# Performance work log

Measured on AMD Instinct MI355X. Metric: run time of the kernel, lower is better.

## Reference

```python
import math
import jax, jax.numpy as jnp
import numpy as np

B, N, DQ, DK, DV, H = 8, 1024, 256, 256, 256, 8
EPS_SM = 1e-15
EPS_LN = 1e-5


def _layer_norm(x, g, b):
    mu = jnp.mean(x, axis=-1, keepdims=True)
    var = jnp.mean((x - mu) ** 2, axis=-1, keepdims=True)
    return (x - mu) * jax.lax.rsqrt(var + EPS_LN) * g + b


def setup_inputs() -> dict:
    key = jax.random.key(0)
    ks = jax.random.split(key, 16)
    s = 0.05
    inp = {
        "Q": jax.random.normal(ks[0], (B, N, DQ), jnp.float32),
        "K": jax.random.normal(ks[1], (B, N, DK), jnp.float32),
        "lengths": jnp.clip(jax.random.randint(ks[2], (B,), 0, N), 1, N),
        "Wq": jax.random.normal(ks[3], (DQ, DV), jnp.float32) * s,
        "bq": jnp.zeros((DV,), jnp.float32),
        "Wk": jax.random.normal(ks[4], (DK, DV), jnp.float32) * s,
        "bk": jnp.zeros((DV,), jnp.float32),
        "Wv": jax.random.normal(ks[5], (DK, DV), jnp.float32) * s,
        "bv": jnp.zeros((DV,), jnp.float32),
        "Wo": jax.random.normal(ks[6], (DV, DV), jnp.float32) * s,
        "bo": jnp.zeros((DV,), jnp.float32),
        "g0": jnp.ones((DV,), jnp.float32),
        "b0": jnp.zeros((DV,), jnp.float32),
        "g1": jnp.ones((DV,), jnp.float32),
        "b1": jnp.zeros((DV,), jnp.float32),
    }
    return inp


def reference(Q, K, lengths, Wq, bq, Wk, bk, Wv, bv, Wo, bo, g0, b0, g1, b1):
    d = DV // H  # head dim
    mask = (jnp.arange(N) < lengths[:, None]).astype(Q.dtype)  # (B, N)
    q = (Q @ Wq + bq) * mask[..., None]  # (B, N, DV)
    k = (K @ Wk + bk) * mask[..., None]
    v = (K @ Wv + bv) * mask[..., None]
    qh = q.reshape(B, N, H, d)
    kh = k.reshape(B, N, H, d)
    vh = v.reshape(B, N, H, d)
    # NB: original scales by sqrt(dim_V), not sqrt(head_dim)
    scores = jnp.einsum("bnhd,bmhd->bhnm", qh, kh) / math.sqrt(DV)
    # set_softmax: raw exp, mask rows and cols by lengths, normalize over keys
    e = jnp.exp(scores) * mask[:, None, :, None] * mask[:, None, None, :]
    A = e / (jnp.sum(e, axis=-1, keepdims=True) + EPS_SM)  # (B, H, N, N)
    O = qh + jnp.einsum("bhnm,bmhd->bnhd", A, vh)  # residual per head
    O = O.reshape(B, N, DV)
    O = _layer_norm(O, g0, b0)
    O = O + jax.nn.relu(O @ Wo + bo)
    O = _layer_norm(O, g1, b1)
    return O
```

## Files before the change

kernel.cpp:

```cpp
#include <hip/hip_runtime.h>
#include <hip/hip_bf16.h>


typedef __attribute__((ext_vector_type(8))) short short8;
typedef __attribute__((ext_vector_type(4))) short short4v;
typedef __attribute__((ext_vector_type(4))) float f32x4;

__device__ __forceinline__ short f2bf(float f) {
    union { float f; unsigned u; } x; x.f = f;
    unsigned r = x.u + 0x7fffu + ((x.u >> 16) & 1u);
    return (short)(r >> 16);
}
__device__ __forceinline__ float bf2f(short s) {
    union { unsigned u; float f; } x; x.u = ((unsigned)(unsigned short)s) << 16;
    return x.f;
}

__global__ __launch_bounds__(256) void wtrans_kernel(
    const float* __restrict__ Wq, const float* __restrict__ Wk,
    const float* __restrict__ Wv, const float* __restrict__ Wo,
    short* __restrict__ WqT, short* __restrict__ WkT,
    short* __restrict__ WvT, short* __restrict__ WoT)
{
    __shared__ short tile[64][72];
    const float* W; short* T;
    switch (blockIdx.y) {
        case 0:  W = Wq; T = WqT; break;
        case 1:  W = Wk; T = WkT; break;
        case 2:  W = Wv; T = WvT; break;
        default: W = Wo; T = WoT; break;
    }
    const int k0 = (blockIdx.x >> 2) * 64;
    const int n0 = (blockIdx.x & 3) * 64;
    const int c  = threadIdx.x & 63;
    const int r4 = threadIdx.x >> 6;
    #pragma unroll
    for (int i = 0; i < 16; i++) {
        int k = r4 + i * 4;
        tile[k][c] = f2bf(W[(size_t)(k0 + k) * 256 + n0 + c]);
    }
    __syncthreads();
    #pragma unroll
    for (int i = 0; i < 16; i++) {
        int n = r4 + i * 4;
        T[(size_t)(n0 + n) * 256 + k0 + c] = tile[c][n];
    }
}

__global__ __launch_bounds__(256) void proj_kernel(
    const float* __restrict__ Q, const float* __restrict__ Kin,
    const short* __restrict__ WqT, const short* __restrict__ WkT, const short* __restrict__ WvT,
    const float* __restrict__ bq, const float* __restrict__ bk, const float* __restrict__ bv,
    const int* __restrict__ lengths,
    short* __restrict__ qb, short* __restrict__ kb, short* __restrict__ vT)
{
    __shared__ short Xt[32][264];
    const int which = blockIdx.y;
    const float* A   = (which == 0) ? Q   : Kin;
    const short* WTa = (which == 0) ? WqT : WkT;

    const int tid = threadIdx.x;
    const int b = blockIdx.x >> 5;
    const int len = lengths[b];
    const int r0b = blockIdx.x * 32;
    const int ntok0b = r0b & 1023;

    if (ntok0b < len) {
        #pragma unroll
        for (int it = 0; it < 8; it++) {
            int e = tid + it * 256;
            int row = e >> 6, c4 = (e & 63) * 4;
            float4 f = *(const float4*)(A + (size_t)(r0b + row) * 256 + c4);
            short4v s4;
            s4[0] = f2bf(f.x); s4[1] = f2bf(f.y); s4[2] = f2bf(f.z); s4[3] = f2bf(f.w);
            *(short4v*)(&Xt[row][c4]) = s4;
        }
    }
    __syncthreads();

    const int lane = tid & 63, wid = tid >> 6;
    const int m = lane & 15, quad = lane >> 4;
    const int rh = wid >> 1, ch = wid & 1;
    const int c0 = ch * 128;
    const int ntok0 = ntok0b + rh * 16;

    f32x4 accA[8], accB[8];
    #pragma unroll
    for (int t = 0; t < 8; t++) {
        accA[t] = (f32x4){0.f, 0.f, 0.f, 0.f};
        accB[t] = (f32x4){0.f, 0.f, 0.f, 0.f};
    }

    if (ntok0 < len) {
        for (int kk = 0; kk < 256; kk += 32) {
            short8 af = *(const short8*)(&Xt[rh * 16 + m][kk + quad * 8]);
            #pragma unroll
            for (int t = 0; t < 8; t++) {
                short8 bfa = *(const short8*)(WTa + (c0 + t * 16 + m) * 256 + kk + quad * 8);
                accA[t] = __builtin_amdgcn_mfma_f32_16x16x32_bf16(af, bfa, accA[t], 0, 0, 0);
            }
            if (which == 1) {
                #pragma unroll
                for (int t = 0; t < 8; t++) {
                    short8 bfb = *(const short8*)(WvT + (c0 + t * 16 + m) * 256 + kk + quad * 8);
                    accB[t] = __builtin_amdgcn_mfma_f32_16x16x32_bf16(af, bfb, accB[t], 0, 0, 0);
                }
            }
        }
    }

    const float KSCALE = 0.0625f;
    #pragma unroll
    for (int t = 0; t < 8; t++) {
        int n = c0 + t * 16 + m;
        int h = n >> 5, i = n & 31;
        int bh = b * 8 + h;
        if (which == 0) {
            float bias = bq[n];
            #pragma unroll
            for (int reg = 0; reg < 4; reg++) {
                int ntok = ntok0 + quad * 4 + reg;
                float val = (ntok < len) ? (accA[t][reg] + bias) : 0.f;
                qb[((size_t)bh * 1024 + ntok) * 32 + i] = f2bf(val);
            }
        } else {
            float bk_ = bk[n];
            float bv_ = bv[n];
            #pragma unroll
            for (int reg = 0; reg < 4; reg++) {
                int ntok = ntok0 + quad * 4 + reg;
                bool ok = ntok < len;
                float vk = ok ? (accA[t][reg] + bk_) * KSCALE : 0.f;
                float vv = ok ? (accB[t][reg] + bv_) : 0.f;
                kb[((size_t)bh * 1024 + ntok) * 32 + i] = f2bf(vk);
                vT[(size_t)(bh * 32 + i) * 1024 + ntok] = f2bf(vv);
            }
        }
    }
}

__global__ __launch_bounds__(256) void attn_kernel(
    const short* __restrict__ qb, const short* __restrict__ kb, const short* __restrict__ vT,
    const int* __restrict__ lengths, float* __restrict__ O1)
{
    __shared__ short Kb[2][64][36];
    __shared__ short Vb[2][32][76];
    __shared__ short P[4][16][72];
    const int tid = threadIdx.x;
    const int lane = tid & 63, wid = tid >> 6;
    const int m = lane & 15, quad = lane >> 4;
    const int bh = blockIdx.y;
    const int b = bh >> 3, h = bh & 7;
    const int len = lengths[b];
    const int qr0 = blockIdx.x * 64 + wid * 16;
    const bool active = qr0 < len;

    const short* qbase = qb + (size_t)bh * 1024 * 32;
    const short* kbase = kb + (size_t)bh * 1024 * 32;
    const short* vbase = vT + (size_t)bh * 32 * 1024;

    const short8 qf = *(const short8*)(qbase + (qr0 + m) * 32 + quad * 8);

    f32x4 o0 = (f32x4){0.f, 0.f, 0.f, 0.f};
    f32x4 o1 = (f32x4){0.f, 0.f, 0.f, 0.f};
    float l[4] = {0.f, 0.f, 0.f, 0.f};

    const int nch = (blockIdx.x * 64 < len) ? ((len + 63) >> 6) : 0;

    short8 kr, vr;
    if (nch > 0) {
        kr = *(const short8*)(kbase + tid * 8);
        vr = *(const short8*)(vbase + (size_t)(tid >> 3) * 1024 + (tid & 7) * 8);
    }

    for (int ci = 0; ci < nch; ci++) {
        const int buf = ci & 1;
        *(short8*)(&Kb[buf][tid >> 2][(tid & 3) * 8]) = kr;
        *(short8*)(&Vb[buf][tid >> 3][(tid & 7) * 8]) = vr;
        if (ci + 1 < nch) {
            int k1 = (ci + 1) * 64;
            kr = *(const short8*)(kbase + k1 * 32 + tid * 8);
            vr = *(const short8*)(vbase + (size_t)(tid >> 3) * 1024 + k1 + (tid & 7) * 8);
        }
        __syncthreads();

        if (active) {
            const int key0 = ci * 64;
            #pragma unroll
            for (int t = 0; t < 4; t++) {
                short8 kf = *(const short8*)(&Kb[buf][t * 16 + m][quad * 8]);
                f32x4 s = __builtin_amdgcn_mfma_f32_16x16x32_bf16(qf, kf,
                            (f32x4){0.f, 0.f, 0.f, 0.f}, 0, 0, 0);
                int col = key0 + t * 16 + m;
                bool cm = col < len;
                #pragma unroll
                for (int reg = 0; reg < 4; reg++) {
                    float e = cm ? __expf(s[reg]) : 0.f;
                    l[reg] += e;
                    P[wid][quad * 4 + reg][t * 16 + m] = f2bf(e);
                }
            }
            asm volatile("s_waitcnt lgkmcnt(0)" ::: "memory");
            #pragma unroll
            for (int c = 0; c < 2; c++) {
                short8 pf  = *(const short8*)(&P[wid][m][c * 32 + quad * 8]);
                short8 vf0 = *(const short8*)(&Vb[buf][m][c * 32 + quad * 8]);
                short8 vf1 = *(const short8*)(&Vb[buf][16 + m][c * 32 + quad * 8]);
                o0 = __builtin_amdgcn_mfma_f32_16x16x32_bf16(pf, vf0, o0, 0, 0, 0);
                o1 = __builtin_amdgcn_mfma_f32_16x16x32_bf16(pf, vf1, o1, 0, 0, 0);
            }
        }
    }

    #pragma unroll
    for (int reg = 0; reg < 4; reg++) {
        float s = l[reg];
        s += __shfl_xor(s, 1); s += __shfl_xor(s, 2);
        s += __shfl_xor(s, 4); s += __shfl_xor(s, 8);
        l[reg] = s;
    }

    const int hbase = h * 32;
    #pragma unroll
    for (int reg = 0; reg < 4; reg++) {
        int qrow = qr0 + quad * 4 + reg;
        float f = (qrow < len) ? 1.f / (l[reg] + 1e-15f) : 0.f;
        size_t obase = ((size_t)(b * 1024 + qrow)) * 256 + hbase;
        float q0 = bf2f(qbase[qrow * 32 + m]);
        float q1 = bf2f(qbase[qrow * 32 + 16 + m]);
        O1[obase + m]      = q0 + o0[reg] * f;
        O1[obase + 16 + m] = q1 + o1[reg] * f;
    }
}

__global__ __launch_bounds__(256) void out_kernel(
    const float* __restrict__ O1, const short* __restrict__ WoT,
    const float* __restrict__ g0, const float* __restrict__ b0,
    const float* __restrict__ bo, const float* __restrict__ g1, const float* __restrict__ b1,
    float* __restrict__ out)
{
    __shared__ short Xs[16][264];
    __shared__ float st[4][2][16];
    const int tid = threadIdx.x;
    const int r0 = blockIdx.x * 16;

    {
        const int lrow  = tid >> 4;
        const int cbase = (tid & 15) * 16;
        const float* rowp = O1 + (size_t)(r0 + lrow) * 256 + cbase;
        float4 a0 = ((const float4*)rowp)[0];
        float4 a1 = ((const float4*)rowp)[1];
        float4 a2 = ((const float4*)rowp)[2];
        float4 a3 = ((const float4*)rowp)[3];
        float s  = a0.x + a0.y + a0.z + a0.w + a1.x + a1.y + a1.z + a1.w
                 + a2.x + a2.y + a2.z + a2.w + a3.x + a3.y + a3.z + a3.w;
        float s2 = a0.x*a0.x + a0.y*a0.y + a0.z*a0.z + a0.w*a0.w
                 + a1.x*a1.x + a1.y*a1.y + a1.z*a1.z + a1.w*a1.w
                 + a2.x*a2.x + a2.y*a2.y + a2.z*a2.z + a2.w*a2.w
                 + a3.x*a3.x + a3.y*a3.y + a3.z*a3.z + a3.w*a3.w;
        s  += __shfl_xor(s, 1);  s  += __shfl_xor(s, 2);
        s  += __shfl_xor(s, 4);  s  += __shfl_xor(s, 8);
        s2 += __shfl_xor(s2, 1); s2 += __shfl_xor(s2, 2);
        s2 += __shfl_xor(s2, 4); s2 += __shfl_xor(s2, 8);
        float mean = s * (1.f / 256.f);
        float var  = s2 * (1.f / 256.f) - mean * mean;
        float rs = rsqrtf(var + 1e-5f);
        float4 g0a = ((const float4*)(g0 + cbase))[0];
        float4 g0b = ((const float4*)(g0 + cbase))[1];
        float4 g0c = ((const float4*)(g0 + cbase))[2];
        float4 g0d = ((const float4*)(g0 + cbase))[3];
        float4 b0a = ((const float4*)(b0 + cbase))[0];
        float4 b0b = ((const float4*)(b0 + cbase))[1];
        float4 b0c = ((const float4*)(b0 + cbase))[2];
        float4 b0d = ((const float4*)(b0 + cbase))[3];
        short8 y0, y1;
        y0[0] = f2bf((a0.x - mean) * rs * g0a.x + b0a.x);
        y0[1] = f2bf((a0.y - mean) * rs * g0a.y + b0a.y);
        y0[2] = f2bf((a0.z - mean) * rs * g0a.z + b0a.z);
        y0[3] = f2bf((a0.w - mean) * rs * g0a.w + b0a.w);
        y0[4] = f2bf((a1.x - mean) * rs * g0b.x + b0b.x);
        y0[5] = f2bf((a1.y - mean) * rs * g0b.y + b0b.y);
        y0[6] = f2bf((a1.z - mean) * rs * g0b.z + b0b.z);
        y0[7] = f2bf((a1.w - mean) * rs * g0b.w + b0b.w);
        y1[0] = f2bf((a2.x - mean) * rs * g0c.x + b0c.x);
        y1[1] = f2bf((a2.y - mean) * rs * g0c.y + b0c.y);
        y1[2] = f2bf((a2.z - mean) * rs * g0c.z + b0c.z);
        y1[3] = f2bf((a2.w - mean) * rs * g0c.w + b0c.w);
        y1[4] = f2bf((a3.x - mean) * rs * g0d.x + b0d.x);
        y1[5] = f2bf((a3.y - mean) * rs * g0d.y + b0d.y);
        y1[6] = f2bf((a3.z - mean) * rs * g0d.z + b0d.z);
        y1[7] = f2bf((a3.w - mean) * rs * g0d.w + b0d.w);
        *(short8*)(&Xs[lrow][cbase])     = y0;
        *(short8*)(&Xs[lrow][cbase + 8]) = y1;
    }
    __syncthreads();

    const int lane = tid & 63, wid = tid >> 6;
    const int m = lane & 15, quad = lane >> 4;
    const int c0 = wid * 64;

    f32x4 acc[4];
    #pragma unroll
    for (int t = 0; t < 4; t++) acc[t] = (f32x4){0.f, 0.f, 0.f, 0.f};

    for (int kk = 0; kk < 256; kk += 32) {
        short8 af = *(const short8*)(&Xs[m][kk + quad * 8]);
        #pragma unroll
        for (int t = 0; t < 4; t++) {
            short8 bf = *(const short8*)(WoT + (c0 + t * 16 + m) * 256 + kk + quad * 8);
            acc[t] = __builtin_amdgcn_mfma_f32_16x16x32_bf16(af, bf, acc[t], 0, 0, 0);
        }
    }

    float s1[4] = {0.f, 0.f, 0.f, 0.f};
    float s2v[4] = {0.f, 0.f, 0.f, 0.f};
    #pragma unroll
    for (int t = 0; t < 4; t++) {
        int n = c0 + t * 16 + m;
        float bon = bo[n];
        #pragma unroll
        for (int reg = 0; reg < 4; reg++) {
            int r = quad * 4 + reg;
            float xv = bf2f(Xs[r][n]);
            float c = acc[t][reg] + bon;
            float yv = xv + (c > 0.f ? c : 0.f);
            acc[t][reg] = yv;
            s1[reg] += yv;
            s2v[reg] += yv * yv;
        }
    }
    #pragma unroll
    for (int reg = 0; reg < 4; reg++) {
        float a = s1[reg], bsum = s2v[reg];
        a += __shfl_xor(a, 1); a += __shfl_xor(a, 2); a += __shfl_xor(a, 4); a += __shfl_xor(a, 8);
        bsum += __shfl_xor(bsum, 1); bsum += __shfl_xor(bsum, 2); bsum += __shfl_xor(bsum, 4); bsum += __shfl_xor(bsum, 8);
        s1[reg] = a; s2v[reg] = bsum;
    }
    if (m == 0) {
        #pragma unroll
        for (int reg = 0; reg < 4; reg++) {
            st[wid][0][quad * 4 + reg] = s1[reg];
            st[wid][1][quad * 4 + reg] = s2v[reg];
        }
    }
    __syncthreads();
    #pragma unroll
    for (int reg = 0; reg < 4; reg++) {
        int r = quad * 4 + reg;
        float t1 = st[0][0][r] + st[1][0][r] + st[2][0][r] + st[3][0][r];
        float t2 = st[0][1][r] + st[1][1][r] + st[2][1][r] + st[3][1][r];
        float mean = t1 * (1.f / 256.f);
        float var  = t2 * (1.f / 256.f) - mean * mean;
        float rs = rsqrtf(var + 1e-5f);
        int token = r0 + r;
        #pragma unroll
        for (int t = 0; t < 4; t++) {
            int n = c0 + t * 16 + m;
            out[(size_t)token * 256 + n] = (acc[t][reg] - mean) * rs * g1[n] + b1[n];
        }
    }
}

extern "C" void kernel_launch(void* const* d_in, const int* in_sizes, int n_in,
                              void* d_out, int out_size, void* d_ws, size_t ws_size,
                              hipStream_t stream) {
    const float* Q   = (const float*)d_in[0];
    const float* K   = (const float*)d_in[1];
    const int* lengths = (const int*)d_in[2];
    const float* Wq  = (const float*)d_in[3];
    const float* bq  = (const float*)d_in[4];
    const float* Wk  = (const float*)d_in[5];
    const float* bk  = (const float*)d_in[6];
    const float* Wv  = (const float*)d_in[7];
    const float* bv  = (const float*)d_in[8];
    const float* Wo  = (const float*)d_in[9];
    const float* bo  = (const float*)d_in[10];
    const float* g0  = (const float*)d_in[11];
    const float* b0  = (const float*)d_in[12];
    const float* g1  = (const float*)d_in[13];
    const float* b1  = (const float*)d_in[14];
    float* out = (float*)d_out;

    char* ws = (char*)d_ws;
    short* qb  = (short*)(ws);
    short* kb  = (short*)(ws + (4u << 20));
    short* vT  = (short*)(ws + (8u << 20));
    float* O1  = (float*)(ws + (12u << 20));
    short* WqT = (short*)(ws + (20u << 20));
    short* WkT = (short*)(ws + (20u << 20) + (128u << 10));
    short* WvT = (short*)(ws + (20u << 20) + (256u << 10));
    short* WoT = (short*)(ws + (20u << 20) + (384u << 10));

    wtrans_kernel<<<dim3(16, 4), 256, 0, stream>>>(Wq, Wk, Wv, Wo, WqT, WkT, WvT, WoT);
    proj_kernel<<<dim3(256, 2), 256, 0, stream>>>(Q, K, WqT, WkT, WvT, bq, bk, bv,
                                                  lengths, qb, kb, vT);
    attn_kernel<<<dim3(16, 64), 256, 0, stream>>>(qb, kb, vT, lengths, O1);
    out_kernel<<<dim3(512), 256, 0, stream>>>(O1, WoT, g0, b0, bo, g1, b1, out);
}
```

Before: 150.7 us.

## Double rows per warp in attention and output kernels to reuse K/V and Wo

The attention kernel now has each warp handle 32 query rows (two 16-row tiles) instead of 16, so each block covers 128 queries and every staged K/V chunk is reused across twice as many rows, halving the grid. The output kernel likewise processes 32 tokens per block, reusing each Wo fragment for two MFMA row tiles. This cuts redundant global loads of K/V and Wo and the number of blocks, at the cost of more registers per thread and less parallelism (512 attention blocks, 256 output blocks), which may hurt occupancy and load balance for short sequences.

```diff
diff --git a/kernel.cpp b/kernel.cpp
--- a/kernel.cpp
+++ b/kernel.cpp
@@ -145,27 +145,30 @@
 {
     __shared__ short Kb[2][64][36];
     __shared__ short Vb[2][32][76];
-    __shared__ short P[4][16][72];
+    __shared__ short P[4][2][16][72];
     const int tid = threadIdx.x;
     const int lane = tid & 63, wid = tid >> 6;
     const int m = lane & 15, quad = lane >> 4;
     const int bh = blockIdx.y;
     const int b = bh >> 3, h = bh & 7;
     const int len = lengths[b];
-    const int qr0 = blockIdx.x * 64 + wid * 16;
-    const bool active = qr0 < len;
+    const int qr0 = blockIdx.x * 128 + wid * 32;
+    const bool act0 = qr0 < len;
+    const bool act1 = qr0 + 16 < len;
 
     const short* qbase = qb + (size_t)bh * 1024 * 32;
     const short* kbase = kb + (size_t)bh * 1024 * 32;
     const short* vbase = vT + (size_t)bh * 32 * 1024;
 
-    const short8 qf = *(const short8*)(qbase + (qr0 + m) * 32 + quad * 8);
-
-    f32x4 o0 = (f32x4){0.f, 0.f, 0.f, 0.f};
-    f32x4 o1 = (f32x4){0.f, 0.f, 0.f, 0.f};
-    float l[4] = {0.f, 0.f, 0.f, 0.f};
-
-    const int nch = (blockIdx.x * 64 < len) ? ((len + 63) >> 6) : 0;
+    const short8 qf0 = *(const short8*)(qbase + (qr0 + m) * 32 + quad * 8);
+    const short8 qf1 = *(const short8*)(qbase + (qr0 + 16 + m) * 32 + quad * 8);
+
+    f32x4 o00 = (f32x4){0.f,0.f,0.f,0.f}, o01 = (f32x4){0.f,0.f,0.f,0.f};
+    f32x4 o10 = (f32x4){0.f,0.f,0.f,0.f}, o11 = (f32x4){0.f,0.f,0.f,0.f};
+    float l0[4] = {0.f,0.f,0.f,0.f};
+    float l1[4] = {0.f,0.f,0.f,0.f};
+
+    const int nch = (blockIdx.x * 128 < len) ? ((len + 63) >> 6) : 0;
 
     short8 kr, vr;
     if (nch > 0) {
@@ -184,52 +187,91 @@
         }
         __syncthreads();
 
-        if (active) {
-            const int key0 = ci * 64;
+        const int key0 = ci * 64;
+        if (act0) {
             #pragma unroll
             for (int t = 0; t < 4; t++) {
                 short8 kf = *(const short8*)(&Kb[buf][t * 16 + m][quad * 8]);
-                f32x4 s = __builtin_amdgcn_mfma_f32_16x16x32_bf16(qf, kf,
+                f32x4 s = __builtin_amdgcn_mfma_f32_16x16x32_bf16(qf0, kf,
                             (f32x4){0.f, 0.f, 0.f, 0.f}, 0, 0, 0);
                 int col = key0 + t * 16 + m;
                 bool cm = col < len;
                 #pragma unroll
                 for (int reg = 0; reg < 4; reg++) {
                     float e = cm ? __expf(s[reg]) : 0.f;
-                    l[reg] += e;
-                    P[wid][quad * 4 + reg][t * 16 + m] = f2bf(e);
+                    l0[reg] += e;
+                    P[wid][0][quad * 4 + reg][t * 16 + m] = f2bf(e);
                 }
             }
             asm volatile("s_waitcnt lgkmcnt(0)" ::: "memory");
             #pragma unroll
             for (int c = 0; c < 2; c++) {
-                short8 pf  = *(const short8*)(&P[wid][m][c * 32 + quad * 8]);
+                short8 pf  = *(const short8*)(&P[wid][0][m][c * 32 + quad * 8]);
                 short8 vf0 = *(const short8*)(&Vb[buf][m][c * 32 + quad * 8]);
                 short8 vf1 = *(const short8*)(&Vb[buf][16 + m][c * 32 + quad * 8]);
-                o0 = __builtin_amdgcn_mfma_f32_16x16x32_bf16(pf, vf0, o0, 0, 0, 0);
-                o1 = __builtin_amdgcn_mfma_f32_16x16x32_bf16(pf, vf1, o1, 0, 0, 0);
+                o00 = __builtin_amdgcn_mfma_f32_16x16x32_bf16(pf, vf0, o00, 0, 0, 0);
+                o01 = __builtin_amdgcn_mfma_f32_16x16x32_bf16(pf, vf1, o01, 0, 0, 0);
+            }
+        }
+        if (act1) {
+            #pragma unroll
+            for (int t = 0; t < 4; t++) {
+                short8 kf = *(const short8*)(&Kb[buf][t * 16 + m][quad * 8]);
+                f32x4 s = __builtin_amdgcn_mfma_f32_16x16x32_bf16(qf1, kf,
+                            (f32x4){0.f, 0.f, 0.f, 0.f}, 0, 0, 0);
+                int col = key0 + t * 16 + m;
+                bool cm = col < len;
+                #pragma unroll
+                for (int reg = 0; reg < 4; reg++) {
+                    float e = cm ? __expf(s[reg]) : 0.f;
+                    l1[reg] += e;
+                    P[wid][1][quad * 4 + reg][t * 16 + m] = f2bf(e);
+                }
+            }
+            asm volatile("s_waitcnt lgkmcnt(0)" ::: "memory");
+            #pragma unroll
+            for (int c = 0; c < 2; c++) {
+                short8 pf  = *(const short8*)(&P[wid][1][m][c * 32 + quad * 8]);
+                short8 vf0 = *(const short8*)(&Vb[buf][m][c * 32 + quad * 8]);
+                short8 vf1 = *(const short8*)(&Vb[buf][16 + m][c * 32 + quad * 8]);
+                o10 = __builtin_amdgcn_mfma_f32_16x16x32_bf16(pf, vf0, o10, 0, 0, 0);
+                o11 = __builtin_amdgcn_mfma_f32_16x16x32_bf16(pf, vf1, o11, 0, 0, 0);
             }
         }
     }
 
     #pragma unroll
     for (int reg = 0; reg < 4; reg++) {
-        float s = l[reg];
+        float s = l0[reg];
         s += __shfl_xor(s, 1); s += __shfl_xor(s, 2);
         s += __shfl_xor(s, 4); s += __shfl_xor(s, 8);
-        l[reg] = s;
+        l0[reg] = s;
+        float u = l1[reg];
+        u += __shfl_xor(u, 1); u += __shfl_xor(u, 2);
+        u += __shfl_xor(u, 4); u += __shfl_xor(u, 8);
+        l1[reg] = u;
     }
 
     const int hbase = h * 32;
     #pragma unroll
     for (int reg = 0; reg < 4; reg++) {
         int qrow = qr0 + quad * 4 + reg;
-        float f = (qrow < len) ? 1.f / (l[reg] + 1e-15f) : 0.f;
+        float f = (qrow < len) ? 1.f / (l0[reg] + 1e-15f) : 0.f;
         size_t obase = ((size_t)(b * 1024 + qrow)) * 256 + hbase;
         float q0 = bf2f(qbase[qrow * 32 + m]);
         float q1 = bf2f(qbase[qrow * 32 + 16 + m]);
-        O1[obase + m]      = q0 + o0[reg] * f;
-        O1[obase + 16 + m] = q1 + o1[reg] * f;
+        O1[obase + m]      = q0 + o00[reg] * f;
+        O1[obase + 16 + m] = q1 + o01[reg] * f;
+    }
+    #pragma unroll
+    for (int reg = 0; reg < 4; reg++) {
+        int qrow = qr0 + 16 + quad * 4 + reg;
+        float f = (qrow < len) ? 1.f / (l1[reg] + 1e-15f) : 0.f;
+        size_t obase = ((size_t)(b * 1024 + qrow)) * 256 + hbase;
+        float q0 = bf2f(qbase[qrow * 32 + m]);
+        float q1 = bf2f(qbase[qrow * 32 + 16 + m]);
+        O1[obase + m]      = q0 + o10[reg] * f;
+        O1[obase + 16 + m] = q1 + o11[reg] * f;
     }
 }
 
@@ -239,59 +281,40 @@
     const float* __restrict__ bo, const float* __restrict__ g1, const float* __restrict__ b1,
     float* __restrict__ out)
 {
-    __shared__ short Xs[16][264];
-    __shared__ float st[4][2][16];
+    __shared__ short Xs[32][264];
+    __shared__ float st[4][2][32];
     const int tid = threadIdx.x;
-    const int r0 = blockIdx.x * 16;
+    const int r0 = blockIdx.x * 32;
 
     {
-        const int lrow  = tid >> 4;
-        const int cbase = (tid & 15) * 16;
+        const int lrow  = tid >> 3;
+        const int cbase = (tid & 7) * 32;
         const float* rowp = O1 + (size_t)(r0 + lrow) * 256 + cbase;
-        float4 a0 = ((const float4*)rowp)[0];
-        float4 a1 = ((const float4*)rowp)[1];
-        float4 a2 = ((const float4*)rowp)[2];
-        float4 a3 = ((const float4*)rowp)[3];
-        float s  = a0.x + a0.y + a0.z + a0.w + a1.x + a1.y + a1.z + a1.w
-                 + a2.x + a2.y + a2.z + a2.w + a3.x + a3.y + a3.z + a3.w;
-        float s2 = a0.x*a0.x + a0.y*a0.y + a0.z*a0.z + a0.w*a0.w
-                 + a1.x*a1.x + a1.y*a1.y + a1.z*a1.z + a1.w*a1.w
-                 + a2.x*a2.x + a2.y*a2.y + a2.z*a2.z + a2.w*a2.w
-                 + a3.x*a3.x + a3.y*a3.y + a3.z*a3.z + a3.w*a3.w;
-        s  += __shfl_xor(s, 1);  s  += __shfl_xor(s, 2);
-        s  += __shfl_xor(s, 4);  s  += __shfl_xor(s, 8);
-        s2 += __shfl_xor(s2, 1); s2 += __shfl_xor(s2, 2);
-        s2 += __shfl_xor(s2, 4); s2 += __shfl_xor(s2, 8);
+        float4 a[8];
+        #pragma unroll
+        for (int j = 0; j < 8; j++) a[j] = ((const float4*)rowp)[j];
+        float s = 0.f, s2 = 0.f;
+        #pragma unroll
+        for (int j = 0; j < 8; j++) {
+            s  += a[j].x + a[j].y + a[j].z + a[j].w;
+            s2 += a[j].x*a[j].x + a[j].y*a[j].y + a[j].z*a[j].z + a[j].w*a[j].w;
+        }
+        s  += __shfl_xor(s, 1);  s  += __shfl_xor(s, 2);  s  += __shfl_xor(s, 4);
+        s2 += __shfl_xor(s2, 1); s2 += __shfl_xor(s2, 2); s2 += __shfl_xor(s2, 4);
         float mean = s * (1.f / 256.f);
         float var  = s2 * (1.f / 256.f) - mean * mean;
         float rs = rsqrtf(var + 1e-5f);
-        float4 g0a = ((const float4*)(g0 + cbase))[0];
-        float4 g0b = ((const float4*)(g0 + cbase))[1];
-        float4 g0c = ((const float4*)(g0 + cbase))[2];
-        float4 g0d = ((const float4*)(g0 + cbase))[3];
-        float4 b0a = ((const float4*)(b0 + cbase))[0];
-        float4 b0b = ((const float4*)(b0 + cbase))[1];
-        float4 b0c = ((const float4*)(b0 + cbase))[2];
-        float4 b0d = ((const float4*)(b0 + cbase))[3];
-        short8 y0, y1;
-        y0[0] = f2bf((a0.x - mean) * rs * g0a.x + b0a.x);
-        y0[1] = f2bf((a0.y - mean) * rs * g0a.y + b0a.y);
-        y0[2] = f2bf((a0.z - mean) * rs * g0a.z + b0a.z);
-        y0[3] = f2bf((a0.w - mean) * rs * g0a.w + b0a.w);
-        y0[4] = f2bf((a1.x - mean) * rs * g0b.x + b0b.x);
-        y0[5] = f2bf((a1.y - mean) * rs * g0b.y + b0b.y);
-        y0[6] = f2bf((a1.z - mean) * rs * g0b.z + b0b.z);
-        y0[7] = f2bf((a1.w - mean) * rs * g0b.w + b0b.w);
-        y1[0] = f2bf((a2.x - mean) * rs * g0c.x + b0c.x);
-        y1[1] = f2bf((a2.y - mean) * rs * g0c.y + b0c.y);
-        y1[2] = f2bf((a2.z - mean) * rs * g0c.z + b0c.z);
-        y1[3] = f2bf((a2.w - mean) * rs * g0c.w + b0c.w);
-        y1[4] = f2bf((a3.x - mean) * rs * g0d.x + b0d.x);
-        y1[5] = f2bf((a3.y - mean) * rs * g0d.y + b0d.y);
-        y1[6] = f2bf((a3.z - mean) * rs * g0d.z + b0d.z);
-        y1[7] = f2bf((a3.w - mean) * rs * g0d.w + b0d.w);
-        *(short8*)(&Xs[lrow][cbase])     = y0;
-        *(short8*)(&Xs[lrow][cbase + 8]) = y1;
+        #pragma unroll
+        for (int j = 0; j < 8; j++) {
+            float4 g = ((const float4*)(g0 + cbase))[j];
+            float4 bb = ((const float4*)(b0 + cbase))[j];
+            short4v y;
+            y[0] = f2bf((a[j].x - mean) * rs * g.x + bb.x);
+            y[1] = f2bf((a[j].y - mean) * rs * g.y + bb.y);
+            y[2] = f2bf((a[j].z - mean) * rs * g.z + bb.z);
+            y[3] = f2bf((a[j].w - mean) * rs * g.w + bb.w);
+            *(short4v*)(&Xs[lrow][cbase + j * 4]) = y;
+        }
     }
     __syncthreads();
 
@@ -299,21 +322,26 @@
     const int m = lane & 15, quad = lane >> 4;
     const int c0 = wid * 64;
 
-    f32x4 acc[4];
-    #pragma unroll
-    for (int t = 0; t < 4; t++) acc[t] = (f32x4){0.f, 0.f, 0.f, 0.f};
+    f32x4 acc0[4], acc1[4];
+    #pragma unroll
+    for (int t = 0; t < 4; t++) {
+        acc0[t] = (f32x4){0.f, 0.f, 0.f, 0.f};
+        acc1[t] = (f32x4){0.f, 0.f, 0.f, 0.f};
+    }
 
     for (int kk = 0; kk < 256; kk += 32) {
-        short8 af = *(const short8*)(&Xs[m][kk + quad * 8]);
+        short8 af0 = *(const short8*)(&Xs[m][kk + quad * 8]);
+        short8 af1 = *(const short8*)(&Xs[16 + m][kk + quad * 8]);
         #pragma unroll
         for (int t = 0; t < 4; t++) {
             short8 bf = *(const short8*)(WoT + (c0 + t * 16 + m) * 256 + kk + quad * 8);
-            acc[t] = __builtin_amdgcn_mfma_f32_16x16x32_bf16(af, bf, acc[t], 0, 0, 0);
-        }
-    }
-
-    float s1[4] = {0.f, 0.f, 0.f, 0.f};
-    float s2v[4] = {0.f, 0.f, 0.f, 0.f};
+            acc0[t] = __builtin_amdgcn_mfma_f32_16x16x32_bf16(af0, bf, acc0[t], 0, 0, 0);
+            acc1[t] = __builtin_amdgcn_mfma_f32_16x16x32_bf16(af1, bf, acc1[t], 0, 0, 0);
+        }
+    }
+
+    float s1[2][4] = {{0.f,0.f,0.f,0.f},{0.f,0.f,0.f,0.f}};
+    float s2v[2][4] = {{0.f,0.f,0.f,0.f},{0.f,0.f,0.f,0.f}};
     #pragma unroll
     for (int t = 0; t < 4; t++) {
         int n = c0 + t * 16 + m;
@@ -321,42 +349,55 @@
         #pragma unroll
         for (int reg = 0; reg < 4; reg++) {
             int r = quad * 4 + reg;
-            float xv = bf2f(Xs[r][n]);
-            float c = acc[t][reg] + bon;
-            float yv = xv + (c > 0.f ? c : 0.f);
-            acc[t][reg] = yv;
-            s1[reg] += yv;
-            s2v[reg] += yv * yv;
-        }
-    }
-    #pragma unroll
-    for (int reg = 0; reg < 4; reg++) {
-        float a = s1[reg], bsum = s2v[reg];
-        a += __shfl_xor(a, 1); a += __shfl_xor(a, 2); a += __shfl_xor(a, 4); a += __shfl_xor(a, 8);
-        bsum += __shfl_xor(bsum, 1); bsum += __shfl_xor(bsum, 2); bsum += __shfl_xor(bsum, 4); bsum += __shfl_xor(bsum, 8);
-        s1[reg] = a; s2v[reg] = bsum;
+            float xv0 = bf2f(Xs[r][n]);
+            float c0v = acc0[t][reg] + bon;
+            float yv0 = xv0 + (c0v > 0.f ? c0v : 0.f);
+            acc0[t][reg] = yv0;
+            s1[0][reg] += yv0;  s2v[0][reg] += yv0 * yv0;
+            float xv1 = bf2f(Xs[16 + r][n]);
+            float c1v = acc1[t][reg] + bon;
+            float yv1 = xv1 + (c1v > 0.f ? c1v : 0.f);
+            acc1[t][reg] = yv1;
+            s1[1][reg] += yv1;  s2v[1][reg] += yv1 * yv1;
+        }
+    }
+    #pragma unroll
+    for (int sub = 0; sub < 2; sub++) {
+        #pragma unroll
+        for (int reg = 0; reg < 4; reg++) {
+            float a = s1[sub][reg], bsum = s2v[sub][reg];
+            a += __shfl_xor(a, 1); a += __shfl_xor(a, 2); a += __shfl_xor(a, 4); a += __shfl_xor(a, 8);
+            bsum += __shfl_xor(bsum, 1); bsum += __shfl_xor(bsum, 2); bsum += __shfl_xor(bsum, 4); bsum += __shfl_xor(bsum, 8);
+            s1[sub][reg] = a; s2v[sub][reg] = bsum;
+        }
     }
     if (m == 0) {
         #pragma unroll
+        for (int sub = 0; sub < 2; sub++)
+            #pragma unroll
+            for (int reg = 0; reg < 4; reg++) {
+                st[wid][0][sub * 16 + quad * 4 + reg] = s1[sub][reg];
+                st[wid][1][sub * 16 + quad * 4 + reg] = s2v[sub][reg];
+            }
+    }
+    __syncthreads();
+    #pragma unroll
+    for (int sub = 0; sub < 2; sub++) {
+        #pragma unroll
         for (int reg = 0; reg < 4; reg++) {
-            st[wid][0][quad * 4 + reg] = s1[reg];
-            st[wid][1][quad * 4 + reg] = s2v[reg];
-        }
-    }
-    __syncthreads();
-    #pragma unroll
-    for (int reg = 0; reg < 4; reg++) {
-        int r = quad * 4 + reg;
-        float t1 = st[0][0][r] + st[1][0][r] + st[2][0][r] + st[3][0][r];
-        float t2 = st[0][1][r] + st[1][1][r] + st[2][1][r] + st[3][1][r];
-        float mean = t1 * (1.f / 256.f);
-        float var  = t2 * (1.f / 256.f) - mean * mean;
-        float rs = rsqrtf(var + 1e-5f);
-        int token = r0 + r;
-        #pragma unroll
-        for (int t = 0; t < 4; t++) {
-            int n = c0 + t * 16 + m;
-            out[(size_t)token * 256 + n] = (acc[t][reg] - mean) * rs * g1[n] + b1[n];
+            int r = sub * 16 + quad * 4 + reg;
+            float t1 = st[0][0][r] + st[1][0][r] + st[2][0][r] + st[3][0][r];
+            float t2 = st[0][1][r] + st[1][1][r] + st[2][1][r] + st[3][1][r];
+            float mean = t1 * (1.f / 256.f);
+            float var  = t2 * (1.f / 256.f) - mean * mean;
+            float rs = rsqrtf(var + 1e-5f);
+            int token = r0 + r;
+            #pragma unroll
+            for (int t = 0; t < 4; t++) {
+                int n = c0 + t * 16 + m;
+                float yv = (sub == 0) ? acc0[t][reg] : acc1[t][reg];
+                out[(size_t)token * 256 + n] = (yv - mean) * rs * g1[n] + b1[n];
+            }
         }
     }
 }
@@ -394,6 +435,6 @@
     wtrans_kernel<<<dim3(16, 4), 256, 0, stream>>>(Wq, Wk, Wv, Wo, WqT, WkT, WvT, WoT);
     proj_kernel<<<dim3(256, 2), 256, 0, stream>>>(Q, K, WqT, WkT, WvT, bq, bk, bv,
                                                   lengths, qb, kb, vT);
-    attn_kernel<<<dim3(16, 64), 256, 0, stream>>>(qb, kb, vT, lengths, O1);
-    out_kernel<<<dim3(512), 256, 0, stream>>>(O1, WoT, g0, b0, bo, g1, b1, out);
-}
+    attn_kernel<<<dim3(8, 64), 256, 0, stream>>>(qb, kb, vT, lengths, O1);
+    out_kernel<<<dim3(256), 256, 0, stream>>>(O1, WoT, g0, b0, bo, g1, b1, out);
+}
```

Measured after the change: 161.2 us. 1.07x slower.
